# Kernel optimization log

Hardware: AMD Instinct MI355X
Metric: run time of the kernel (lower is better)

## Reference

```python
import jax, jax.numpy as jnp
import numpy as np

LN_EPS = 1e-5


def layer_norm(x, gamma, beta):
    mu = jnp.mean(x, axis=-1, keepdims=True)
    var = jnp.mean(jnp.square(x - mu), axis=-1, keepdims=True)
    return (x - mu) * jax.lax.rsqrt(var + LN_EPS) * gamma + beta


def setup_inputs() -> dict:
    key = jax.random.key(0)
    ks = jax.random.split(key, 7)
    B, S, D = 8, 1024, 512
    H, Dh = 8, 64
    scale = 1.0 / np.sqrt(D)
    x = jax.random.normal(ks[0], (B, S, D), dtype=jnp.float32)
    Wq = jax.random.normal(ks[1], (D, H * Dh), dtype=jnp.float32) * scale
    Wk = jax.random.normal(ks[2], (D, H * Dh), dtype=jnp.float32) * scale
    Wv = jax.random.normal(ks[3], (D, H * Dh), dtype=jnp.float32) * scale
    Wfc = jax.random.normal(ks[4], (H * Dh, D), dtype=jnp.float32) * scale
    gamma = jnp.ones((D,), dtype=jnp.float32)
    beta = jnp.zeros((D,), dtype=jnp.float32)
    return {"x": x, "Wq": Wq, "Wk": Wk, "Wv": Wv, "Wfc": Wfc, "gamma": gamma, "beta": beta}


def reference(x, Wq, Wk, Wv, Wfc, gamma, beta):
    B, S, D = x.shape
    H, Dh = 8, 64
    Q = (x @ Wq).reshape(B, S, H, Dh).transpose(0, 2, 1, 3)  # [B,H,S,Dh]
    K = (x @ Wk).reshape(B, S, H, Dh).transpose(0, 2, 1, 3)
    V = (x @ Wv).reshape(B, S, H, Dh).transpose(0, 2, 1, 3)
    scores = jnp.einsum('bhqd,bhkd->bhqk', Q, K) / np.sqrt(Dh).astype(np.float32)
    # tridiagonal band mask; NOTE: original fills off-band with -1e-09 (not -inf)
    idx = jnp.arange(S)
    band = jnp.abs(idx[:, None] - idx[None, :]) <= 1  # [S,S]
    scores = jnp.where(band, scores, jnp.float32(-1e-09))
    attn = jax.nn.softmax(scores, axis=-1)
    context = jnp.einsum('bhqk,bhkd->bhqd', attn, V)  # [B,H,S,Dh]
    context = context.transpose(0, 2, 1, 3).reshape(B, S, H * Dh)
    out = context @ Wfc
    return layer_norm(out + x, gamma, beta)
```

## Files before the change

### kernel.cpp

```cpp
#include <hip/hip_runtime.h>
#include <math.h>


typedef short     s8v  __attribute__((ext_vector_type(8)));
typedef float     f4v  __attribute__((ext_vector_type(4)));
typedef unsigned short us4v __attribute__((ext_vector_type(4)));
typedef unsigned short us8v __attribute__((ext_vector_type(8)));

__device__ __forceinline__ unsigned short f2b(float f) {
  union { float f; unsigned int u; } v; v.f = f;
  unsigned int u = v.u;
  return (unsigned short)((u + 0x7fffu + ((u >> 16) & 1u)) >> 16);
}
__device__ __forceinline__ float b2f(unsigned short u) {
  union { unsigned int i; float f; } v; v.i = ((unsigned int)u) << 16;
  return v.f;
}
__device__ __forceinline__ void gload_lds16(const void* g, void* l) {
  __builtin_amdgcn_global_load_lds(
      (const __attribute__((address_space(1))) void*)g,
      (__attribute__((address_space(3))) void*)l, 16, 0, 0);
}

__global__ __launch_bounds__(256) void conv_kernel(
    const float* __restrict__ x,
    const float* __restrict__ Wq, const float* __restrict__ Wk,
    const float* __restrict__ Wv, const float* __restrict__ Wfc,
    unsigned short* __restrict__ xb, unsigned short* __restrict__ Wt,
    float* __restrict__ Vsum) {
  __shared__ unsigned short tile[32][33];
  const int bid = blockIdx.x, t = threadIdx.x;
  if (bid < 4096) {
    const int i = bid * 256 + t;
    const float4 f = ((const float4*)x)[i];
    us4v o; o[0] = f2b(f.x); o[1] = f2b(f.y); o[2] = f2b(f.z); o[3] = f2b(f.w);
    ((us4v*)xb)[i] = o;
  } else if (bid < 5120) {
    const int id = bid - 4096;
    const int z = id >> 8, rem = id & 255;
    const int bx = rem & 15, by = rem >> 4;
    const float* W = (z == 0) ? Wq : (z == 1) ? Wk : (z == 2) ? Wv : Wfc;
    const int tx = t & 31, ty = t >> 5;
    const int n0 = bx * 32, k0 = by * 32;
    #pragma unroll
    for (int r = ty; r < 32; r += 8)
      tile[r][tx] = f2b(W[(size_t)(k0 + r) * 512 + n0 + tx]);
    __syncthreads();
    unsigned short* dst = Wt + (size_t)z * 512 * 512;
    #pragma unroll
    for (int r = ty; r < 32; r += 8)
      dst[(size_t)(n0 + r) * 512 + k0 + tx] = tile[tx][r];
  } else {
    float4 zz = {0.f, 0.f, 0.f, 0.f};
    #pragma unroll
    for (int p = 0; p < 4; ++p) ((float4*)Vsum)[p * 256 + t] = zz;
  }
}

__global__ __launch_bounds__(256) void gemm_qkv_kernel(
    const unsigned short* __restrict__ A, const unsigned short* __restrict__ Bt,
    unsigned short* __restrict__ C, float* __restrict__ Vsum) {
  const int N = 1536, K = 512;
  __shared__ __align__(16) unsigned short smem[16384];
  unsigned short* As = smem;
  unsigned short* Bs = smem + 8192;
  const int t = threadIdx.x, wave = t >> 6, lane = t & 63;
  const int wr = wave >> 1, wc = wave & 1;
  const int quad = lane >> 4, l16 = lane & 15;
  const int bm = blockIdx.y * 128, bn = blockIdx.x * 128;

  const unsigned short *gA[4], *gB[4];
  #pragma unroll
  for (int p = 0; p < 4; ++p) {
    const int ci = wave * 256 + p * 64 + lane;
    const int r = ci >> 3, c = (ci & 7) ^ (r & 7);
    gA[p] = A + (size_t)(bm + r) * K + c * 8;
    gB[p] = Bt + (size_t)(bn + r) * K + c * 8;
  }

  f4v acc[4][4];
  #pragma unroll
  for (int i = 0; i < 4; ++i)
    #pragma unroll
    for (int j = 0; j < 4; ++j) {
      f4v z = {0.f, 0.f, 0.f, 0.f};
      acc[i][j] = z;
    }

  #pragma unroll
  for (int it = 0; it < 8; ++it) {
    const int kt = it * 64;
    #pragma unroll
    for (int p = 0; p < 4; ++p)
      gload_lds16(gA[p] + kt, As + wave * 2048 + p * 512);
    #pragma unroll
    for (int p = 0; p < 4; ++p)
      gload_lds16(gB[p] + kt, Bs + wave * 2048 + p * 512);
    __syncthreads();

    #pragma unroll
    for (int s = 0; s < 2; ++s) {
      s8v af[4], bf[4];
      #pragma unroll
      for (int i = 0; i < 4; ++i) {
        const int r = wr * 64 + i * 16 + l16;
        af[i] = *(const s8v*)&As[(r * 8 + ((quad + 4 * s) ^ (r & 7))) * 8];
      }
      #pragma unroll
      for (int j = 0; j < 4; ++j) {
        const int r = wc * 64 + j * 16 + l16;
        bf[j] = *(const s8v*)&Bs[(r * 8 + ((quad + 4 * s) ^ (r & 7))) * 8];
      }
      #pragma unroll
      for (int i = 0; i < 4; ++i)
        #pragma unroll
        for (int j = 0; j < 4; ++j)
          acc[i][j] = __builtin_amdgcn_mfma_f32_16x16x32_bf16(
              af[i], bf[j], acc[i][j], 0, 0, 0);
    }
    __syncthreads();
  }

  if (bn >= 1024) {
    const int b = bm >> 10;
    #pragma unroll
    for (int j = 0; j < 4; ++j) {
      float ps = 0.f;
      #pragma unroll
      for (int i = 0; i < 4; ++i)
        #pragma unroll
        for (int r = 0; r < 4; ++r) ps += acc[i][j][r];
      ps += __shfl_xor(ps, 16);
      ps += __shfl_xor(ps, 32);
      if (quad == 0)
        atomicAdd(&Vsum[b * 512 + (bn - 1024) + wc * 64 + j * 16 + l16], ps);
    }
  }

  #pragma unroll
  for (int i = 0; i < 4; ++i) {
    const int lr0 = wr * 64 + i * 16 + quad * 4;
    #pragma unroll
    for (int j = 0; j < 4; ++j) {
      const int lc = wc * 64 + j * 16 + l16;
      #pragma unroll
      for (int r = 0; r < 4; ++r)
        smem[(lr0 + r) * 128 + lc] = f2b(acc[i][j][r]);
    }
  }
  __syncthreads();
  #pragma unroll
  for (int p = 0; p < 8; ++p) {
    const int row = p * 16 + (t >> 4);
    const int ch  = t & 15;
    *(us8v*)(C + (size_t)(bm + row) * N + bn + ch * 8) =
        *(const us8v*)&smem[row * 128 + ch * 8];
  }
}

#define KVS 68
__global__ __launch_bounds__(256) void attn_kernel(
    const unsigned short* __restrict__ QKV, const float* __restrict__ Vsum,
    unsigned short* __restrict__ ctx) {
  __shared__ __align__(16) unsigned short Qs[130 * KVS];
  __shared__ __align__(16) unsigned short Ks[130 * KVS];
  __shared__ __align__(16) unsigned short Vs[130 * KVS];
  __shared__ __align__(16) float vs_s[64];
  const int bh = blockIdx.x;
  const int b = bh >> 3, h = bh & 7;
  const int q0 = blockIdx.y * 128;
  const int t = threadIdx.x;
  const size_t rowb = ((size_t)b * 1024) * 1536;

  #pragma unroll
  for (int p = 0; p < 5; ++p) {
    const int i = p * 32 + (t >> 3);
    if (i < 130) {
      int g = q0 - 1 + i;
      g = g < 0 ? 0 : (g > 1023 ? 1023 : g);
      const unsigned short* src =
          QKV + rowb + (size_t)g * 1536 + h * 64 + (t & 7) * 8;
      const us8v qv = *(const us8v*)(src);
      const us8v kv = *(const us8v*)(src + 512);
      const us8v vv = *(const us8v*)(src + 1024);
      us4v lo, hi;
      #pragma unroll
      for (int r = 0; r < 4; ++r) { lo[r] = qv[r]; hi[r] = qv[r + 4]; }
      *(us4v*)&Qs[i * KVS + (t & 7) * 8]     = lo;
      *(us4v*)&Qs[i * KVS + (t & 7) * 8 + 4] = hi;
      #pragma unroll
      for (int r = 0; r < 4; ++r) { lo[r] = kv[r]; hi[r] = kv[r + 4]; }
      *(us4v*)&Ks[i * KVS + (t & 7) * 8]     = lo;
      *(us4v*)&Ks[i * KVS + (t & 7) * 8 + 4] = hi;
      #pragma unroll
      for (int r = 0; r < 4; ++r) { lo[r] = vv[r]; hi[r] = vv[r + 4]; }
      *(us4v*)&Vs[i * KVS + (t & 7) * 8]     = lo;
      *(us4v*)&Vs[i * KVS + (t & 7) * 8 + 4] = hi;
    }
  }
  if (t < 64) vs_s[t] = Vsum[(b << 9) + h * 64 + t];
  __syncthreads();

  const int q    = q0 + (t >> 1);
  const int half = t & 1;
  const int li   = (t >> 1) + 1;
  const int co   = half * 32;

  float pm = 0.f, p0 = 0.f, pp = 0.f;
  #pragma unroll
  for (int jj = 0; jj < 8; ++jj) {
    const us4v qv = *(const us4v*)&Qs[li * KVS + co + jj * 4];
    const us4v km = *(const us4v*)&Ks[(li - 1) * KVS + co + jj * 4];
    const us4v k0 = *(const us4v*)&Ks[li * KVS + co + jj * 4];
    const us4v kp = *(const us4v*)&Ks[(li + 1) * KVS + co + jj * 4];
    #pragma unroll
    for (int r = 0; r < 4; ++r) {
      const float qf = b2f(qv[r]);
      pm += qf * b2f(km[r]);
      p0 += qf * b2f(k0[r]);
      pp += qf * b2f(kp[r]);
    }
  }
  pm += __shfl_xor(pm, 1);
  p0 += __shfl_xor(p0, 1);
  pp += __shfl_xor(pp, 1);

  const float OFF = -1e-9f;
  const float s0 = p0 * 0.125f;
  const float sm = (q > 0)    ? pm * 0.125f : OFF;
  const float sp = (q < 1023) ? pp * 0.125f : OFF;
  const float m  = fmaxf(fmaxf(s0, sm), fmaxf(sp, OFF));
  const float e0 = __expf(s0 - m), em = __expf(sm - m), ep = __expf(sp - m);
  const float eoff = __expf(OFF - m);
  const float inv  = 1.f / (e0 + em + ep + 1021.f * eoff);
  const float wm = (em - eoff) * inv, w0 = (e0 - eoff) * inv,
              wp = (ep - eoff) * inv, wt = eoff * inv;

  unsigned short* cp = ctx + ((size_t)(b * 1024 + q)) * 512 + h * 64 + co;
  #pragma unroll
  for (int jj = 0; jj < 8; ++jj) {
    const us4v a  = *(const us4v*)&Vs[(li - 1) * KVS + co + jj * 4];
    const us4v v0 = *(const us4v*)&Vs[li * KVS + co + jj * 4];
    const us4v c  = *(const us4v*)&Vs[(li + 1) * KVS + co + jj * 4];
    const float4 vsv = *(const float4*)&vs_s[co + jj * 4];
    us4v o;
    o[0] = f2b(wt * vsv.x + wm * b2f(a[0]) + w0 * b2f(v0[0]) + wp * b2f(c[0]));
    o[1] = f2b(wt * vsv.y + wm * b2f(a[1]) + w0 * b2f(v0[1]) + wp * b2f(c[1]));
    o[2] = f2b(wt * vsv.z + wm * b2f(a[2]) + w0 * b2f(v0[2]) + wp * b2f(c[2]));
    o[3] = f2b(wt * vsv.w + wm * b2f(a[3]) + w0 * b2f(v0[3]) + wp * b2f(c[3]));
    *(us4v*)(cp + jj * 4) = o;
  }
}

#define OS 516

__global__ __launch_bounds__(512) void gemm_fcln_kernel(
    const unsigned short* __restrict__ A,
    const unsigned short* __restrict__ Bt,
    const unsigned short* __restrict__ xb, const float* __restrict__ gamma,
    const float* __restrict__ beta, float* __restrict__ y) {
  const int K = 512;
  __shared__ __align__(16) unsigned short smem[69632];
  float* outS = (float*)smem;

  const int t = threadIdx.x, wave = t >> 6, lane = t & 63;
  const int wrr = wave >> 2, wcc = wave & 3;
  const int quad = lane >> 4, l16 = lane & 15;
  const int bm = blockIdx.x * 32;

  const int ciA = wave * 64 + lane;
  const int rA = ciA >> 3, cA = (ciA & 7) ^ (rA & 7);
  const unsigned short* gA = A + (size_t)(bm + rA) * K + cA * 8;
  const unsigned short* gB[8];
  #pragma unroll
  for (int p = 0; p < 8; ++p) {
    const int ci = wave * 512 + p * 64 + lane;
    const int r = ci >> 3, c = (ci & 7) ^ (r & 7);
    gB[p] = Bt + (size_t)r * K + c * 8;
  }

  f4v acc[8];
  #pragma unroll
  for (int j = 0; j < 8; ++j) {
    f4v z = {0.f, 0.f, 0.f, 0.f};
    acc[j] = z;
  }

  if (wave < 4) gload_lds16(gA, smem + wave * 512);
  #pragma unroll
  for (int p = 0; p < 8; ++p)
    gload_lds16(gB[p], smem + 2048 + wave * 4096 + p * 512);
  __syncthreads();

  #pragma unroll
  for (int it = 0; it < 8; ++it) {
    const int cur = (it & 1) * 34816;
    const int nxt = 34816 - cur;
    const unsigned short* Ab = smem + cur;
    const unsigned short* Bb = smem + cur + 2048;
    const int rm = wrr * 16 + l16;
    const s8v af0 = *(const s8v*)&Ab[(rm * 8 + (quad ^ (rm & 7))) * 8];
    const s8v af1 = *(const s8v*)&Ab[(rm * 8 + ((quad + 4) ^ (rm & 7))) * 8];
    s8v bf0[8];
    #pragma unroll
    for (int j = 0; j < 8; ++j) {
      const int n = wcc * 128 + j * 16 + l16;
      bf0[j] = *(const s8v*)&Bb[(n * 8 + (quad ^ (n & 7))) * 8];
    }
    if (it < 7) {
      const int kt = (it + 1) * 64;
      if (wave < 4) gload_lds16(gA + kt, smem + nxt + wave * 512);
      #pragma unroll
      for (int p = 0; p < 8; ++p)
        gload_lds16(gB[p] + kt, smem + nxt + 2048 + wave * 4096 + p * 512);
    }
    #pragma unroll
    for (int j = 0; j < 8; ++j)
      acc[j] = __builtin_amdgcn_mfma_f32_16x16x32_bf16(af0, bf0[j], acc[j], 0, 0, 0);
    #pragma unroll
    for (int j = 0; j < 8; ++j) {
      const int n = wcc * 128 + j * 16 + l16;
      const s8v bf1 = *(const s8v*)&Bb[(n * 8 + ((quad + 4) ^ (n & 7))) * 8];
      acc[j] = __builtin_amdgcn_mfma_f32_16x16x32_bf16(af1, bf1, acc[j], 0, 0, 0);
    }
    __syncthreads();
  }

  #pragma unroll
  for (int j = 0; j < 8; ++j) {
    const int col = wcc * 128 + j * 16 + l16;
    const int row0 = wrr * 16 + quad * 4;
    #pragma unroll
    for (int r = 0; r < 4; ++r)
      outS[(row0 + r) * OS + col] = acc[j][r];
  }
  __syncthreads();

  const int row = t >> 4, l = t & 15;
  const size_t gbase = (size_t)(bm + row) * 512;
  float4 v[8];
  float s1 = 0.f, s2 = 0.f;
  #pragma unroll
  for (int k = 0; k < 8; ++k) {
    const int c = k * 64 + l * 4;
    const float4 a = *(const float4*)&outS[row * OS + c];
    const us4v xv = *(const us4v*)&xb[gbase + c];
    float4 w;
    w.x = a.x + b2f(xv[0]); w.y = a.y + b2f(xv[1]);
    w.z = a.z + b2f(xv[2]); w.w = a.w + b2f(xv[3]);
    v[k] = w;
    s1 += w.x + w.y + w.z + w.w;
    s2 += w.x * w.x + w.y * w.y + w.z * w.z + w.w * w.w;
  }
  #pragma unroll
  for (int m = 1; m < 16; m <<= 1) {
    s1 += __shfl_xor(s1, m);
    s2 += __shfl_xor(s2, m);
  }
  const float mu  = s1 * (1.f / 512.f);
  const float var = s2 * (1.f / 512.f) - mu * mu;
  const float rs  = rsqrtf(var + 1e-5f);
  #pragma unroll
  for (int k = 0; k < 8; ++k) {
    const int c = k * 64 + l * 4;
    const float4 g  = *(const float4*)&gamma[c];
    const float4 bb = *(const float4*)&beta[c];
    float4 o;
    o.x = (v[k].x - mu) * rs * g.x + bb.x;
    o.y = (v[k].y - mu) * rs * g.y + bb.y;
    o.z = (v[k].z - mu) * rs * g.z + bb.z;
    o.w = (v[k].w - mu) * rs * g.w + bb.w;
    *(float4*)&y[gbase + c] = o;
  }
}

extern "C" void kernel_launch(void* const* d_in, const int* in_sizes, int n_in,
                              void* d_out, int out_size, void* d_ws, size_t ws_size,
                              hipStream_t stream) {
  const float* x     = (const float*)d_in[0];
  const float* Wq    = (const float*)d_in[1];
  const float* Wk    = (const float*)d_in[2];
  const float* Wv    = (const float*)d_in[3];
  const float* Wfc   = (const float*)d_in[4];
  const float* gamma = (const float*)d_in[5];
  const float* beta  = (const float*)d_in[6];
  float* y = (float*)d_out;

  char* ws = (char*)d_ws;
  unsigned short* Wt   = (unsigned short*)(ws);
  unsigned short* xb   = (unsigned short*)(ws + 2097152);
  unsigned short* QKV  = (unsigned short*)(ws + 10485760);
  float*          Vsum = (float*)(ws + 35651584);
  unsigned short* ctx  = (unsigned short*)(ws + 35667968);

  conv_kernel<<<5121, 256, 0, stream>>>(x, Wq, Wk, Wv, Wfc, xb, Wt, Vsum);
  gemm_qkv_kernel<<<dim3(12, 64), 256, 0, stream>>>(xb, Wt, QKV, Vsum);
  attn_kernel<<<dim3(64, 8), 256, 0, stream>>>(QKV, Vsum, ctx);
  gemm_fcln_kernel<<<256, 512, 0, stream>>>(
      ctx, Wt + (size_t)1536 * 512, xb, gamma, beta, y);
}
```

Before: 119.9 us.

## Fuse banded attention into the output-projection GEMM with LayerNorm

Removes the separate attention kernel and computes the tridiagonal-softmax context for each 32-row tile directly inside the FC+LayerNorm kernel. The context is written into LDS with an XOR swizzle and used as the A operand, so the ctx buffer no longer makes a round trip through global memory and one launch is dropped. In exchange, each block reads Q/K/V rows straight from global without LDS reuse, so neighbour rows are loaded roughly three times. LDS use per block also grows, which may lower occupancy.

After: 127.7 us. 6.5% more time.

```diff
diff --git a/kernel.cpp b/kernel.cpp
--- a/kernel.cpp
+++ b/kernel.cpp
@@ -158,119 +158,22 @@
   }
 }
 
-#define KVS 68
-__global__ __launch_bounds__(256) void attn_kernel(
-    const unsigned short* __restrict__ QKV, const float* __restrict__ Vsum,
-    unsigned short* __restrict__ ctx) {
-  __shared__ __align__(16) unsigned short Qs[130 * KVS];
-  __shared__ __align__(16) unsigned short Ks[130 * KVS];
-  __shared__ __align__(16) unsigned short Vs[130 * KVS];
-  __shared__ __align__(16) float vs_s[64];
-  const int bh = blockIdx.x;
-  const int b = bh >> 3, h = bh & 7;
-  const int q0 = blockIdx.y * 128;
-  const int t = threadIdx.x;
-  const size_t rowb = ((size_t)b * 1024) * 1536;
-
-  #pragma unroll
-  for (int p = 0; p < 5; ++p) {
-    const int i = p * 32 + (t >> 3);
-    if (i < 130) {
-      int g = q0 - 1 + i;
-      g = g < 0 ? 0 : (g > 1023 ? 1023 : g);
-      const unsigned short* src =
-          QKV + rowb + (size_t)g * 1536 + h * 64 + (t & 7) * 8;
-      const us8v qv = *(const us8v*)(src);
-      const us8v kv = *(const us8v*)(src + 512);
-      const us8v vv = *(const us8v*)(src + 1024);
-      us4v lo, hi;
-      #pragma unroll
-      for (int r = 0; r < 4; ++r) { lo[r] = qv[r]; hi[r] = qv[r + 4]; }
-      *(us4v*)&Qs[i * KVS + (t & 7) * 8]     = lo;
-      *(us4v*)&Qs[i * KVS + (t & 7) * 8 + 4] = hi;
-      #pragma unroll
-      for (int r = 0; r < 4; ++r) { lo[r] = kv[r]; hi[r] = kv[r + 4]; }
-      *(us4v*)&Ks[i * KVS + (t & 7) * 8]     = lo;
-      *(us4v*)&Ks[i * KVS + (t & 7) * 8 + 4] = hi;
-      #pragma unroll
-      for (int r = 0; r < 4; ++r) { lo[r] = vv[r]; hi[r] = vv[r + 4]; }
-      *(us4v*)&Vs[i * KVS + (t & 7) * 8]     = lo;
-      *(us4v*)&Vs[i * KVS + (t & 7) * 8 + 4] = hi;
-    }
-  }
-  if (t < 64) vs_s[t] = Vsum[(b << 9) + h * 64 + t];
-  __syncthreads();
-
-  const int q    = q0 + (t >> 1);
-  const int half = t & 1;
-  const int li   = (t >> 1) + 1;
-  const int co   = half * 32;
-
-  float pm = 0.f, p0 = 0.f, pp = 0.f;
-  #pragma unroll
-  for (int jj = 0; jj < 8; ++jj) {
-    const us4v qv = *(const us4v*)&Qs[li * KVS + co + jj * 4];
-    const us4v km = *(const us4v*)&Ks[(li - 1) * KVS + co + jj * 4];
-    const us4v k0 = *(const us4v*)&Ks[li * KVS + co + jj * 4];
-    const us4v kp = *(const us4v*)&Ks[(li + 1) * KVS + co + jj * 4];
-    #pragma unroll
-    for (int r = 0; r < 4; ++r) {
-      const float qf = b2f(qv[r]);
-      pm += qf * b2f(km[r]);
-      p0 += qf * b2f(k0[r]);
-      pp += qf * b2f(kp[r]);
-    }
-  }
-  pm += __shfl_xor(pm, 1);
-  p0 += __shfl_xor(p0, 1);
-  pp += __shfl_xor(pp, 1);
-
-  const float OFF = -1e-9f;
-  const float s0 = p0 * 0.125f;
-  const float sm = (q > 0)    ? pm * 0.125f : OFF;
-  const float sp = (q < 1023) ? pp * 0.125f : OFF;
-  const float m  = fmaxf(fmaxf(s0, sm), fmaxf(sp, OFF));
-  const float e0 = __expf(s0 - m), em = __expf(sm - m), ep = __expf(sp - m);
-  const float eoff = __expf(OFF - m);
-  const float inv  = 1.f / (e0 + em + ep + 1021.f * eoff);
-  const float wm = (em - eoff) * inv, w0 = (e0 - eoff) * inv,
-              wp = (ep - eoff) * inv, wt = eoff * inv;
-
-  unsigned short* cp = ctx + ((size_t)(b * 1024 + q)) * 512 + h * 64 + co;
-  #pragma unroll
-  for (int jj = 0; jj < 8; ++jj) {
-    const us4v a  = *(const us4v*)&Vs[(li - 1) * KVS + co + jj * 4];
-    const us4v v0 = *(const us4v*)&Vs[li * KVS + co + jj * 4];
-    const us4v c  = *(const us4v*)&Vs[(li + 1) * KVS + co + jj * 4];
-    const float4 vsv = *(const float4*)&vs_s[co + jj * 4];
-    us4v o;
-    o[0] = f2b(wt * vsv.x + wm * b2f(a[0]) + w0 * b2f(v0[0]) + wp * b2f(c[0]));
-    o[1] = f2b(wt * vsv.y + wm * b2f(a[1]) + w0 * b2f(v0[1]) + wp * b2f(c[1]));
-    o[2] = f2b(wt * vsv.z + wm * b2f(a[2]) + w0 * b2f(v0[2]) + wp * b2f(c[2]));
-    o[3] = f2b(wt * vsv.w + wm * b2f(a[3]) + w0 * b2f(v0[3]) + wp * b2f(c[3]));
-    *(us4v*)(cp + jj * 4) = o;
-  }
-}
-
 #define OS 516
 
-__global__ __launch_bounds__(512) void gemm_fcln_kernel(
-    const unsigned short* __restrict__ A,
+__global__ __launch_bounds__(512) void attn_fcln_kernel(
+    const unsigned short* __restrict__ QKV,
+    const float* __restrict__ Vsum,
     const unsigned short* __restrict__ Bt,
     const unsigned short* __restrict__ xb, const float* __restrict__ gamma,
     const float* __restrict__ beta, float* __restrict__ y) {
   const int K = 512;
-  __shared__ __align__(16) unsigned short smem[69632];
+  __shared__ __align__(16) unsigned short smem[81920];
+  unsigned short* ctxS = smem + 65536;
   float* outS = (float*)smem;
 
   const int t = threadIdx.x, wave = t >> 6, lane = t & 63;
-  const int wrr = wave >> 2, wcc = wave & 3;
-  const int quad = lane >> 4, l16 = lane & 15;
   const int bm = blockIdx.x * 32;
 
-  const int ciA = wave * 64 + lane;
-  const int rA = ciA >> 3, cA = (ciA & 7) ^ (rA & 7);
-  const unsigned short* gA = A + (size_t)(bm + rA) * K + cA * 8;
   const unsigned short* gB[8];
   #pragma unroll
   for (int p = 0; p < 8; ++p) {
@@ -278,6 +181,92 @@
     const int r = ci >> 3, c = (ci & 7) ^ (r & 7);
     gB[p] = Bt + (size_t)r * K + c * 8;
   }
+  #pragma unroll
+  for (int p = 0; p < 8; ++p)
+    gload_lds16(gB[p], smem + wave * 4096 + p * 512);
+
+  {
+    const int ql   = t >> 4;
+    const int h    = (t >> 1) & 7;
+    const int half = t & 1;
+    const int b    = bm >> 10;
+    const int qq   = (bm & 1023) + ql;
+    const int co   = h * 64 + half * 32;
+    const size_t rowb = (size_t)b * 1024 * 1536;
+    const int qm = qq > 0 ? qq - 1 : 0;
+    const int qp = qq < 1023 ? qq + 1 : 1023;
+    const unsigned short* Qp  = QKV + rowb + (size_t)qq * 1536 + co;
+    const unsigned short* Kp0 = QKV + rowb + (size_t)qq * 1536 + 512 + co;
+    const unsigned short* Kpm = QKV + rowb + (size_t)qm * 1536 + 512 + co;
+    const unsigned short* Kpp = QKV + rowb + (size_t)qp * 1536 + 512 + co;
+
+    us8v qv[4], km[4], k0[4], kp[4];
+    #pragma unroll
+    for (int j = 0; j < 4; ++j) {
+      qv[j] = *(const us8v*)(Qp  + j * 8);
+      km[j] = *(const us8v*)(Kpm + j * 8);
+      k0[j] = *(const us8v*)(Kp0 + j * 8);
+      kp[j] = *(const us8v*)(Kpp + j * 8);
+    }
+    float pm = 0.f, p0 = 0.f, pp = 0.f;
+    #pragma unroll
+    for (int j = 0; j < 4; ++j)
+      #pragma unroll
+      for (int r = 0; r < 8; ++r) {
+        const float qf = b2f(qv[j][r]);
+        pm += qf * b2f(km[j][r]);
+        p0 += qf * b2f(k0[j][r]);
+        pp += qf * b2f(kp[j][r]);
+      }
+    pm += __shfl_xor(pm, 1);
+    p0 += __shfl_xor(p0, 1);
+    pp += __shfl_xor(pp, 1);
+
+    const float OFF = -1e-9f;
+    const float s0 = p0 * 0.125f;
+    const float sm = (qq > 0)    ? pm * 0.125f : OFF;
+    const float sp = (qq < 1023) ? pp * 0.125f : OFF;
+    const float m  = fmaxf(fmaxf(s0, sm), fmaxf(sp, OFF));
+    const float e0 = __expf(s0 - m), em = __expf(sm - m), ep = __expf(sp - m);
+    const float eoff = __expf(OFF - m);
+    const float inv  = 1.f / (e0 + em + ep + 1021.f * eoff);
+    const float wm = (em - eoff) * inv, w0 = (e0 - eoff) * inv,
+                wp = (ep - eoff) * inv, wt = eoff * inv;
+
+    const unsigned short* Vp0 = Kp0 + 512;
+    const unsigned short* Vpm = Kpm + 512;
+    const unsigned short* Vpp = Kpp + 512;
+    const float* vsp = Vsum + b * 512 + co;
+    us8v o[4];
+    #pragma unroll
+    for (int jj = 0; jj < 4; ++jj) {
+      const us8v a  = *(const us8v*)(Vpm + jj * 8);
+      const us8v v0 = *(const us8v*)(Vp0 + jj * 8);
+      const us8v c  = *(const us8v*)(Vpp + jj * 8);
+      const float4 vsa = *(const float4*)&vsp[jj * 8];
+      const float4 vsb = *(const float4*)&vsp[jj * 8 + 4];
+      #pragma unroll
+      for (int r = 0; r < 4; ++r) {
+        const float vs0 = (&vsa.x)[r];
+        const float vs1 = (&vsb.x)[r];
+        o[jj][r]     = f2b(wt * vs0 + wm * b2f(a[r]) + w0 * b2f(v0[r]) +
+                           wp * b2f(c[r]));
+        o[jj][r + 4] = f2b(wt * vs1 + wm * b2f(a[r + 4]) + w0 * b2f(v0[r + 4]) +
+                           wp * b2f(c[r + 4]));
+      }
+    }
+    #pragma unroll
+    for (int s = 0; s < 4; ++s) {
+      const int jj = (s + h) & 3;
+      const int ch = (co >> 3) + jj;
+      const int slot = (ch & 56) | ((ch & 7) ^ (ql & 7));
+      *(us8v*)&ctxS[ql * 512 + slot * 8] = o[jj];
+    }
+  }
+  __syncthreads();
+
+  const int wrr = wave >> 2, wcc = wave & 3;
+  const int quad = lane >> 4, l16 = lane & 15;
 
   f4v acc[8];
   #pragma unroll
@@ -286,21 +275,16 @@
     acc[j] = z;
   }
 
-  if (wave < 4) gload_lds16(gA, smem + wave * 512);
-  #pragma unroll
-  for (int p = 0; p < 8; ++p)
-    gload_lds16(gB[p], smem + 2048 + wave * 4096 + p * 512);
-  __syncthreads();
-
   #pragma unroll
   for (int it = 0; it < 8; ++it) {
-    const int cur = (it & 1) * 34816;
-    const int nxt = 34816 - cur;
-    const unsigned short* Ab = smem + cur;
-    const unsigned short* Bb = smem + cur + 2048;
+    const int cur = (it & 1) * 32768;
+    const int nxt = 32768 - cur;
+    const unsigned short* Bb = smem + cur;
     const int rm = wrr * 16 + l16;
-    const s8v af0 = *(const s8v*)&Ab[(rm * 8 + (quad ^ (rm & 7))) * 8];
-    const s8v af1 = *(const s8v*)&Ab[(rm * 8 + ((quad + 4) ^ (rm & 7))) * 8];
+    const s8v af0 =
+        *(const s8v*)&ctxS[rm * 512 + (it * 8 + (quad ^ (rm & 7))) * 8];
+    const s8v af1 =
+        *(const s8v*)&ctxS[rm * 512 + (it * 8 + ((quad + 4) ^ (rm & 7))) * 8];
     s8v bf0[8];
     #pragma unroll
     for (int j = 0; j < 8; ++j) {
@@ -309,10 +293,9 @@
     }
     if (it < 7) {
       const int kt = (it + 1) * 64;
-      if (wave < 4) gload_lds16(gA + kt, smem + nxt + wave * 512);
       #pragma unroll
       for (int p = 0; p < 8; ++p)
-        gload_lds16(gB[p] + kt, smem + nxt + 2048 + wave * 4096 + p * 512);
+        gload_lds16(gB[p] + kt, smem + nxt + wave * 4096 + p * 512);
     }
     #pragma unroll
     for (int j = 0; j < 8; ++j)
@@ -391,11 +374,9 @@
   unsigned short* xb   = (unsigned short*)(ws + 2097152);
   unsigned short* QKV  = (unsigned short*)(ws + 10485760);
   float*          Vsum = (float*)(ws + 35651584);
-  unsigned short* ctx  = (unsigned short*)(ws + 35667968);
 
   conv_kernel<<<5121, 256, 0, stream>>>(x, Wq, Wk, Wv, Wfc, xb, Wt, Vsum);
   gemm_qkv_kernel<<<dim3(12, 64), 256, 0, stream>>>(xb, Wt, QKV, Vsum);
-  attn_kernel<<<dim3(64, 8), 256, 0, stream>>>(QKV, Vsum, ctx);
-  gemm_fcln_kernel<<<256, 512, 0, stream>>>(
-      ctx, Wt + (size_t)1536 * 512, xb, gamma, beta, y);
-}
+  attn_fcln_kernel<<<256, 512, 0, stream>>>(
+      QKV, Vsum, Wt + (size_t)1536 * 512, xb, gamma, beta, y);
+}
```
